# Performance work log

Hardware: AMD Instinct MI355X
Metric: run time of the kernel (lower is better)

Reference implementation:

```python
import jax, jax.numpy as jnp
import numpy as np

B, N, EB, NA, DIM, NIT = 256, 128, 5, 64, 512, 3  # EB = n_bonds + 1 (channel 0 = no-bond, dropped)


def setup_inputs() -> dict:
    key = jax.random.key(0)
    ks = jax.random.split(key, 10)
    adj = jax.random.uniform(ks[0], (B, N, N, EB), dtype=jnp.float32)
    node = jax.random.normal(ks[1], (B, N, NA), dtype=jnp.float32)
    hidden = jnp.zeros((B, N, DIM), dtype=jnp.float32)  # accepted but unused by forward
    # nn.Linear default init: U(-1/sqrt(fan_in), 1/sqrt(fan_in))
    se = 1.0 / np.sqrt(NA)
    sd = 1.0 / np.sqrt(DIM)
    W_embed = jax.random.uniform(ks[2], (NA, DIM), minval=-se, maxval=se, dtype=jnp.float32)
    b_embed = jax.random.uniform(ks[3], (DIM,), minval=-se, maxval=se, dtype=jnp.float32)
    W_layers = jax.random.uniform(ks[4], (NIT, DIM, DIM), minval=-sd, maxval=sd, dtype=jnp.float32)
    b_layers = jax.random.uniform(ks[5], (NIT, DIM), minval=-sd, maxval=sd, dtype=jnp.float32)
    W_out = jax.random.uniform(ks[6], (DIM, 1), minval=-sd, maxval=sd, dtype=jnp.float32)
    b_out = jax.random.uniform(ks[7], (1,), minval=-sd, maxval=sd, dtype=jnp.float32)
    return {"adj": adj, "hidden": hidden, "node": node,
            "W_embed": W_embed, "b_embed": b_embed,
            "W_layers": W_layers, "b_layers": b_layers,
            "W_out": W_out, "b_out": b_out}


def reference(adj, hidden, node, W_embed, b_embed, W_layers, b_layers, W_out, b_out):
    # adj[:, :, :, 1:].permute(0, 3, 1, 2) -> [B, E, N, N]
    a = jnp.transpose(adj[..., 1:], (0, 3, 1, 2))
    h = node @ W_embed + b_embed  # [B, N, DIM]
    for i in range(NIT):  # WLSLinearLayer: relu(Linear(h + sum_e adj_e @ h))
        agg = jnp.einsum('benm,bmd->bnd', a, h)  # sum over bond types of neighbor aggregation
        h = jax.nn.relu((h + agg) @ W_layers[i] + b_layers[i])
    graph_repr = jnp.mean(h, axis=1)  # [B, DIM]
    logit = graph_repr @ W_out + b_out  # [B, 1], activation=None path
    return (logit, graph_repr)
```

## Files before the change

kernel.cpp:

```cpp
#include <hip/hip_runtime.h>
#include <hip/hip_bf16.h>


typedef __bf16 bf16;
typedef __bf16 bf16x4 __attribute__((ext_vector_type(4)));
typedef __bf16 bf16x8 __attribute__((ext_vector_type(8)));
typedef float floatx4 __attribute__((ext_vector_type(4)));

#define AS  136

__global__ __launch_bounds__(256) void k_pack(const float* __restrict__ We,
                                              const float* __restrict__ Wl,
                                              bf16* __restrict__ PWe,
                                              bf16* __restrict__ PWl) {
    __shared__ float S[512][17];
    int z = blockIdx.y, td = blockIdx.x;
    const float* src; bf16* dst; int K;
    if (z < 3) { src = Wl + (size_t)z * 262144; dst = PWl + (size_t)z * 262144; K = 512; }
    else       { src = We;                      dst = PWe;                      K = 64; }
    int tid = threadIdx.x;
    int x = tid & 15, y = tid >> 4;
    for (int kb = 0; kb < K; kb += 16) {
        int k = kb + y;
        S[k][x] = src[(size_t)k * 512 + td * 16 + x];
    }
    __syncthreads();
    int lane = tid & 63, w = tid >> 6, q = lane >> 4, l16 = lane & 15;
    int KT = K >> 5;
    for (int tk = w; tk < KT; tk += 4) {
        bf16x8 v;
#pragma unroll
        for (int j = 0; j < 8; j++) v[j] = (bf16)S[tk * 32 + q * 8 + j][l16];
        *(bf16x8*)&dst[(size_t)((td * KT + tk) * 64 + lane) * 8] = v;
    }
}

__global__ __launch_bounds__(1024, 4) void k_mega(
    const float* __restrict__ adj,
    const float* __restrict__ nodef,
    const bf16* __restrict__ PWe,
    const float* __restrict__ b_embed,
    const bf16* __restrict__ PWl,
    const float* __restrict__ b_layers,
    const float* __restrict__ W_out,
    const float* __restrict__ b_out,
    float* __restrict__ out)
{
    __shared__ __align__(16) char pool[137216];
    bf16* HT = (bf16*)pool;

    const int b = blockIdx.x;
    const int tid = threadIdx.x;
    const int lane = tid & 63, wid = tid >> 6;
    const int q = lane >> 4, l16 = lane & 15;

    bf16* AhatL = (bf16*)pool;
    {
        const float4* srcb = (const float4*)(adj + (size_t)b * 81920);
#pragma unroll 2
        for (int p = 0; p < 4; p++) {
            int t = p * 1024 + tid;
            const float4* ptr = srcb + (size_t)t * 5;
            float4 v0 = ptr[0], v1 = ptr[1], v2 = ptr[2], v3 = ptr[3], v4 = ptr[4];
            float s0 = v0.y + v0.z + v0.w + v1.x;
            float s1 = v1.z + v1.w + v2.x + v2.y;
            float s2 = v2.w + v3.x + v3.y + v3.z;
            float s3 = v4.x + v4.y + v4.z + v4.w;
            int n = t >> 5, m0 = (t & 31) * 4;
            bf16x4 o;
            o[0] = (bf16)(s0 + ((n == m0 + 0) ? 1.f : 0.f));
            o[1] = (bf16)(s1 + ((n == m0 + 1) ? 1.f : 0.f));
            o[2] = (bf16)(s2 + ((n == m0 + 2) ? 1.f : 0.f));
            o[3] = (bf16)(s3 + ((n == m0 + 3) ? 1.f : 0.f));
            *(bf16x4*)&AhatL[n * AS + m0] = o;
        }
    }
    __syncthreads();

    const int ntw = wid & 7, dh = wid >> 3;
    bf16x8 ahf[4];
#pragma unroll
    for (int kk = 0; kk < 4; kk++)
        ahf[kk] = *(const bf16x8*)&AhatL[(ntw * 16 + l16) * AS + kk * 32 + q * 8];
    __syncthreads();

    {
        const int wmE = wid >> 3, wnE = wid & 7;
        const float* Ab = nodef + (size_t)b * 8192;
        floatx4 accE[4][4] = {};
#pragma unroll
        for (int kk = 0; kk < 2; kk++) {
            bf16x8 af[4], bfr[4];
#pragma unroll
            for (int mt = 0; mt < 4; mt++) {
                const float* srcp = Ab + (size_t)(wmE * 64 + mt * 16 + l16) * 64 + kk * 32 + q * 8;
                float4 x = *(const float4*)srcp;
                float4 y = *(const float4*)(srcp + 4);
                bf16x8 v;
                v[0] = (bf16)x.x; v[1] = (bf16)x.y; v[2] = (bf16)x.z; v[3] = (bf16)x.w;
                v[4] = (bf16)y.x; v[5] = (bf16)y.y; v[6] = (bf16)y.z; v[7] = (bf16)y.w;
                af[mt] = v;
            }
#pragma unroll
            for (int nt = 0; nt < 4; nt++) {
                int td = wnE * 4 + nt;
                bfr[nt] = *(const bf16x8*)&PWe[(size_t)((td * 2 + kk) * 64 + lane) * 8];
            }
#pragma unroll
            for (int mt = 0; mt < 4; mt++)
#pragma unroll
                for (int nt = 0; nt < 4; nt++)
                    accE[mt][nt] = __builtin_amdgcn_mfma_f32_16x16x32_bf16(af[mt], bfr[nt], accE[mt][nt], 0, 0, 0);
        }
#pragma unroll
        for (int mt = 0; mt < 4; mt++)
#pragma unroll
            for (int nt = 0; nt < 4; nt++) {
                int d = wnE * 64 + nt * 16 + l16;
                float bv = b_embed[d];
                int c = wmE * 8 + mt * 2 + (q >> 1);
                int off = ((c ^ (d & 15)) << 3) + (q & 1) * 4;
                bf16x4 pk;
#pragma unroll
                for (int r = 0; r < 4; r++) pk[r] = (bf16)(accE[mt][nt][r] + bv);
                *(bf16x4*)&HT[d * 128 + off] = pk;
            }
    }
    __syncthreads();

    const int nw = wid & 1, dw = wid >> 1;

    for (int it = 0; it < 3; it++) {
        const bf16* WT = PWl + (size_t)it * 262144;
        const float* bl = b_layers + it * 512;

        floatx4 at[16] = {};
#pragma unroll
        for (int dtile = 0; dtile < 16; dtile++) {
            int drow = dh * 256 + dtile * 16 + l16;
#pragma unroll
            for (int kk = 0; kk < 4; kk++) {
                int off = ((4 * kk + q) ^ (drow & 15)) << 3;
                bf16x8 af = *(const bf16x8*)&HT[drow * 128 + off];
                at[dtile] = __builtin_amdgcn_mfma_f32_16x16x32_bf16(af, ahf[kk], at[dtile], 0, 0, 0);
            }
        }
        __syncthreads();
        {
            int n = ntw * 16 + l16;
#pragma unroll
            for (int dtile = 0; dtile < 16; dtile++) {
                int c = dh * 32 + dtile * 2 + (q >> 1);
                int off = ((c ^ l16) << 3) + (q & 1) * 4;
                bf16x4 pk;
#pragma unroll
                for (int r = 0; r < 4; r++) pk[r] = (bf16)at[dtile][r];
                *(bf16x4*)&HT[n * 512 + off] = pk;
            }
        }
        __syncthreads();

        floatx4 acc[4][4] = {};
        for (int dc = 0; dc < 16; dc++) {
            bf16x8 bfr0 = *(const bf16x8*)&WT[(size_t)(((dw * 4 + 0) * 16 + dc) * 64 + lane) * 8];
            bf16x8 bfr1 = *(const bf16x8*)&WT[(size_t)(((dw * 4 + 1) * 16 + dc) * 64 + lane) * 8];
            bf16x8 af2[4];
#pragma unroll
            for (int mt = 0; mt < 4; mt++) {
                int nn = nw * 64 + mt * 16 + l16;
                int c = (dc * 4 + q) ^ (nn & 15);
                af2[mt] = *(const bf16x8*)&HT[nn * 512 + (c << 3)];
            }
            bf16x8 bfr2 = *(const bf16x8*)&WT[(size_t)(((dw * 4 + 2) * 16 + dc) * 64 + lane) * 8];
#pragma unroll
            for (int mt = 0; mt < 4; mt++)
                acc[mt][0] = __builtin_amdgcn_mfma_f32_16x16x32_bf16(af2[mt], bfr0, acc[mt][0], 0, 0, 0);
            bf16x8 bfr3 = *(const bf16x8*)&WT[(size_t)(((dw * 4 + 3) * 16 + dc) * 64 + lane) * 8];
#pragma unroll
            for (int mt = 0; mt < 4; mt++)
                acc[mt][1] = __builtin_amdgcn_mfma_f32_16x16x32_bf16(af2[mt], bfr1, acc[mt][1], 0, 0, 0);
#pragma unroll
            for (int mt = 0; mt < 4; mt++)
                acc[mt][2] = __builtin_amdgcn_mfma_f32_16x16x32_bf16(af2[mt], bfr2, acc[mt][2], 0, 0, 0);
#pragma unroll
            for (int mt = 0; mt < 4; mt++)
                acc[mt][3] = __builtin_amdgcn_mfma_f32_16x16x32_bf16(af2[mt], bfr3, acc[mt][3], 0, 0, 0);
        }

        if (it < 2) {
            __syncthreads();
#pragma unroll
            for (int nt = 0; nt < 4; nt++) {
                int dp = dw * 64 + nt * 16 + l16;
                float bv = bl[dp];
#pragma unroll
                for (int mt = 0; mt < 4; mt++) {
                    int c = nw * 8 + mt * 2 + (q >> 1);
                    int off = ((c ^ (dp & 15)) << 3) + (q & 1) * 4;
                    bf16x4 pk;
#pragma unroll
                    for (int r = 0; r < 4; r++) pk[r] = (bf16)fmaxf(acc[mt][nt][r] + bv, 0.f);
                    *(bf16x4*)&HT[dp * 128 + off] = pk;
                }
            }
            __syncthreads();
        } else {
            float* RsF = (float*)(pool + 131072);
#pragma unroll
            for (int nt = 0; nt < 4; nt++) {
                int dp = dw * 64 + nt * 16 + l16;
                float bv = bl[dp];
                float s = 0.f;
#pragma unroll
                for (int mt = 0; mt < 4; mt++)
#pragma unroll
                    for (int r = 0; r < 4; r++)
                        s += fmaxf(acc[mt][nt][r] + bv, 0.f);
                s += __shfl_down(s, 32);
                s += __shfl_down(s, 16);
                if (lane < 16) RsF[nw * 512 + dp] = s;
            }
        }
    }
    __syncthreads();

    float* RsF = (float*)(pool + 131072);
    float* lpF = (float*)(pool + 131072 + 4096);
    if (tid < 512) {
        float g = (RsF[tid] + RsF[512 + tid]) * (1.f / 128.f);
        out[256 + (size_t)b * 512 + tid] = g;
        lpF[tid] = g * W_out[tid];
    }
    __syncthreads();
    for (int s = 256; s > 0; s >>= 1) {
        if (tid < s) lpF[tid] += lpF[tid + s];
        __syncthreads();
    }
    if (tid == 0) out[b] = lpF[0] + b_out[0];
}

extern "C" void kernel_launch(void* const* d_in, const int* in_sizes, int n_in,
                              void* d_out, int out_size, void* d_ws, size_t ws_size,
                              hipStream_t stream) {
    const float* adj      = (const float*)d_in[0];
    const float* node     = (const float*)d_in[2];
    const float* W_embed  = (const float*)d_in[3];
    const float* b_embed  = (const float*)d_in[4];
    const float* W_layers = (const float*)d_in[5];
    const float* b_layers = (const float*)d_in[6];
    const float* W_out    = (const float*)d_in[7];
    const float* b_out    = (const float*)d_in[8];
    float* out = (float*)d_out;

    char* ws = (char*)d_ws;
    bf16* PWe = (bf16*)(ws);
    bf16* PWl = (bf16*)(ws + 65536);

    k_pack<<<dim3(32, 4), 256, 0, stream>>>(W_embed, W_layers, PWe, PWl);
    k_mega<<<256, 1024, 0, stream>>>(adj, node, PWe, b_embed, PWl, b_layers,
                                     W_out, b_out, out);
}
```

Baseline: 282.0 us.

## Retile layer GEMM so each wave owns all 128 rows and 32 output columns

Changes the per-wave tile of the dense layer GEMM from 64 rows x 64 columns to 128 rows x 32 columns. Each weight fragment is loaded once per wave and reused across all eight row tiles, and the next K-slice of weights is prefetched one step ahead in registers. The cross-wave partial sum for the final mean reduction goes away, which shrinks shared memory slightly. In exchange, per-wave LDS reads of the activation matrix double while global weight traffic halves.

```diff
diff --git a/kernel.cpp b/kernel.cpp
--- a/kernel.cpp
+++ b/kernel.cpp
@@ -46,7 +46,7 @@
     const float* __restrict__ b_out,
     float* __restrict__ out)
 {
-    __shared__ __align__(16) char pool[137216];
+    __shared__ __align__(16) char pool[135168];
     bf16* HT = (bf16*)pool;
 
     const int b = blockIdx.x;
@@ -128,11 +128,12 @@
     }
     __syncthreads();
 
-    const int nw = wid & 1, dw = wid >> 1;
-
     for (int it = 0; it < 3; it++) {
         const bf16* WT = PWl + (size_t)it * 262144;
         const float* bl = b_layers + it * 512;
+
+        bf16x8 wf0 = *(const bf16x8*)&WT[(size_t)(((wid * 2 + 0) * 16 + 0) * 64 + lane) * 8];
+        bf16x8 wf1 = *(const bf16x8*)&WT[(size_t)(((wid * 2 + 1) * 16 + 0) * 64 + lane) * 8];
 
         floatx4 at[16] = {};
 #pragma unroll
@@ -160,42 +161,44 @@
         }
         __syncthreads();
 
-        floatx4 acc[4][4] = {};
+        floatx4 acc[8][2] = {};
         for (int dc = 0; dc < 16; dc++) {
-            bf16x8 bfr0 = *(const bf16x8*)&WT[(size_t)(((dw * 4 + 0) * 16 + dc) * 64 + lane) * 8];
-            bf16x8 bfr1 = *(const bf16x8*)&WT[(size_t)(((dw * 4 + 1) * 16 + dc) * 64 + lane) * 8];
-            bf16x8 af2[4];
-#pragma unroll
-            for (int mt = 0; mt < 4; mt++) {
-                int nn = nw * 64 + mt * 16 + l16;
-                int c = (dc * 4 + q) ^ (nn & 15);
-                af2[mt] = *(const bf16x8*)&HT[nn * 512 + (c << 3)];
-            }
-            bf16x8 bfr2 = *(const bf16x8*)&WT[(size_t)(((dw * 4 + 2) * 16 + dc) * 64 + lane) * 8];
-#pragma unroll
-            for (int mt = 0; mt < 4; mt++)
-                acc[mt][0] = __builtin_amdgcn_mfma_f32_16x16x32_bf16(af2[mt], bfr0, acc[mt][0], 0, 0, 0);
-            bf16x8 bfr3 = *(const bf16x8*)&WT[(size_t)(((dw * 4 + 3) * 16 + dc) * 64 + lane) * 8];
-#pragma unroll
-            for (int mt = 0; mt < 4; mt++)
-                acc[mt][1] = __builtin_amdgcn_mfma_f32_16x16x32_bf16(af2[mt], bfr1, acc[mt][1], 0, 0, 0);
-#pragma unroll
-            for (int mt = 0; mt < 4; mt++)
-                acc[mt][2] = __builtin_amdgcn_mfma_f32_16x16x32_bf16(af2[mt], bfr2, acc[mt][2], 0, 0, 0);
-#pragma unroll
-            for (int mt = 0; mt < 4; mt++)
-                acc[mt][3] = __builtin_amdgcn_mfma_f32_16x16x32_bf16(af2[mt], bfr3, acc[mt][3], 0, 0, 0);
+            int dcn = (dc + 1) & 15;
+            bf16x8 nf0 = *(const bf16x8*)&WT[(size_t)(((wid * 2 + 0) * 16 + dcn) * 64 + lane) * 8];
+            bf16x8 nf1 = *(const bf16x8*)&WT[(size_t)(((wid * 2 + 1) * 16 + dcn) * 64 + lane) * 8];
+            int c = ((dc * 4 + q) ^ l16) << 3;
+            bf16x8 afa[4];
+#pragma unroll
+            for (int mt = 0; mt < 4; mt++)
+                afa[mt] = *(const bf16x8*)&HT[(mt * 16 + l16) * 512 + c];
+#pragma unroll
+            for (int mt = 0; mt < 4; mt++)
+                acc[mt][0] = __builtin_amdgcn_mfma_f32_16x16x32_bf16(afa[mt], wf0, acc[mt][0], 0, 0, 0);
+#pragma unroll
+            for (int mt = 0; mt < 4; mt++)
+                acc[mt][1] = __builtin_amdgcn_mfma_f32_16x16x32_bf16(afa[mt], wf1, acc[mt][1], 0, 0, 0);
+            bf16x8 afb[4];
+#pragma unroll
+            for (int mt = 0; mt < 4; mt++)
+                afb[mt] = *(const bf16x8*)&HT[((mt + 4) * 16 + l16) * 512 + c];
+#pragma unroll
+            for (int mt = 0; mt < 4; mt++)
+                acc[mt + 4][0] = __builtin_amdgcn_mfma_f32_16x16x32_bf16(afb[mt], wf0, acc[mt + 4][0], 0, 0, 0);
+#pragma unroll
+            for (int mt = 0; mt < 4; mt++)
+                acc[mt + 4][1] = __builtin_amdgcn_mfma_f32_16x16x32_bf16(afb[mt], wf1, acc[mt + 4][1], 0, 0, 0);
+            wf0 = nf0; wf1 = nf1;
         }
 
         if (it < 2) {
             __syncthreads();
 #pragma unroll
-            for (int nt = 0; nt < 4; nt++) {
-                int dp = dw * 64 + nt * 16 + l16;
+            for (int nt = 0; nt < 2; nt++) {
+                int dp = wid * 32 + nt * 16 + l16;
                 float bv = bl[dp];
 #pragma unroll
-                for (int mt = 0; mt < 4; mt++) {
-                    int c = nw * 8 + mt * 2 + (q >> 1);
+                for (int mt = 0; mt < 8; mt++) {
+                    int c = mt * 2 + (q >> 1);
                     int off = ((c ^ (dp & 15)) << 3) + (q & 1) * 4;
                     bf16x4 pk;
 #pragma unroll
@@ -207,27 +210,27 @@
         } else {
             float* RsF = (float*)(pool + 131072);
 #pragma unroll
-            for (int nt = 0; nt < 4; nt++) {
-                int dp = dw * 64 + nt * 16 + l16;
+            for (int nt = 0; nt < 2; nt++) {
+                int dp = wid * 32 + nt * 16 + l16;
                 float bv = bl[dp];
                 float s = 0.f;
 #pragma unroll
-                for (int mt = 0; mt < 4; mt++)
+                for (int mt = 0; mt < 8; mt++)
 #pragma unroll
                     for (int r = 0; r < 4; r++)
                         s += fmaxf(acc[mt][nt][r] + bv, 0.f);
                 s += __shfl_down(s, 32);
                 s += __shfl_down(s, 16);
-                if (lane < 16) RsF[nw * 512 + dp] = s;
+                if (lane < 16) RsF[dp] = s;
             }
         }
     }
     __syncthreads();
 
     float* RsF = (float*)(pool + 131072);
-    float* lpF = (float*)(pool + 131072 + 4096);
+    float* lpF = (float*)(pool + 131072 + 2048);
     if (tid < 512) {
-        float g = (RsF[tid] + RsF[512 + tid]) * (1.f / 128.f);
+        float g = RsF[tid] * (1.f / 128.f);
         out[256 + (size_t)b * 512 + tid] = g;
         lpF[tid] = g * W_out[tid];
     }
```

After: 257.9 us. 1.09x faster.
